# Kernel tuning notes

Measured on AMD Instinct MI355X. Metric: run time of the kernel, lower is better.

Reference implementation:

```python
import jax, jax.numpy as jnp
import numpy as np

REF_CHANNEL = 0
DIAG_EPS = 1e-7   # diag_loading coefficient
TIK_EPS = 1e-8    # additive eps in diagonal loading / trace denominator
MASK_EPS = 1e-15  # PSD mask-normalization eps


def _psd(spec, mask):
    # spec: (b, c, f, t) complex; mask: (b, f, t) real
    # PSD module: normalize mask over time, weight outer products, sum over t.
    m = mask / (mask.sum(axis=-1, keepdims=True) + MASK_EPS)
    return jnp.einsum('bcft,beft,bft->bfce', spec, spec.conj(), m.astype(spec.dtype))


def setup_inputs() -> dict:
    key = jax.random.key(0)
    k1, k2, k3, k4 = jax.random.split(key, 4)
    B, C, F, T = 4, 6, 257, 2000
    return {
        'spec_real': jax.random.normal(k1, (B, C, F, T), dtype=jnp.float32),
        'spec_imag': jax.random.normal(k2, (B, C, F, T), dtype=jnp.float32),
        'mask_s': jax.random.uniform(k3, (B, F, T), dtype=jnp.float32),
        'mask_n': jax.random.uniform(k4, (B, F, T), dtype=jnp.float32),
    }


def reference(spec_real, spec_imag, mask_s, mask_n):
    spec = spec_real + 1j * spec_imag                     # (b, c, f, t) complex64
    C = spec.shape[1]

    psd_s = _psd(spec, mask_s)                            # (b, f, c, c)
    psd_n = _psd(spec, mask_n)                            # (b, f, c, c)

    # Diagonal loading (Tikhonov regularization) of the noise PSD.
    tr_n = jnp.einsum('bfcc->bf', psd_n).real
    epsilon = jax.lax.stop_gradient(tr_n * DIAG_EPS + TIK_EPS)   # torch uses no_grad here
    psd_n = psd_n + epsilon[..., None, None] * jnp.eye(C, dtype=spec.dtype)

    # ref_channel solution: w = (psd_n^-1 psd_s) / trace(psd_n^-1 psd_s) @ u
    numerator = jnp.linalg.solve(psd_n, psd_s)            # (b, f, c, c)
    tr = jnp.einsum('bfcc->bf', numerator)
    ws = numerator / (tr[..., None, None] + TIK_EPS)
    w = ws[..., :, REF_CHANNEL]                           # one-hot u selects column -> (b, f, c)

    # enhanced = w^H Y
    enh = jnp.einsum('bfc,bcft->bft', w.conj(), spec)     # (b, f, t) complex
    return jnp.stack([enh.real, enh.imag], axis=-1)       # (b, f, t, 2) float32
```

## Files before the change

### kernel.cpp

```cpp
#include <hip/hip_runtime.h>

#define NB 4
#define NC 6
#define NF 257
#define NT 2000
#define NG (NB * NF)
#define NPAIR 15
#define NACC 74
#define NCHUNK 2
#define TCH (NT / NCHUNK)
#define NP4 (TCH / 4)
#define BLK 256
#define CS  (NF * NT)
#define CS4 (CS / 4)

typedef float nfloat4 __attribute__((ext_vector_type(4)));

template<int CTRL>
__device__ __forceinline__ float dpp_add(float v) {
    int s = __builtin_amdgcn_update_dpp(0, __builtin_bit_cast(int, v), CTRL, 0xF, 0xF, true);
    return v + __builtin_bit_cast(float, s);
}

__global__ __launch_bounds__(BLK, 4) void psd_kernel(
    const float* __restrict__ sr, const float* __restrict__ si,
    const float* __restrict__ ms, const float* __restrict__ mn,
    float* __restrict__ wsp)
{
    constexpr int PC[NPAIR] = {0,0,0,0,0,1,1,1,1,2,2,2,3,3,4};
    constexpr int PE[NPAIR] = {1,2,3,4,5,2,3,4,5,3,4,5,4,5,5};

    const int bx = blockIdx.x;
    const int g  = bx >> 1;
    const int b  = g / NF;
    const int f  = g - b * NF;
    const int tb = (bx & 1) * TCH;
    const int sbase = b * NC * CS + f * NT + tb;
    const int mbase = g * NT + tb;

    const float4* s4r = (const float4*)(sr + sbase);
    const float4* s4i = (const float4*)(si + sbase);
    const float4* m4s = (const float4*)(ms + mbase);
    const float4* m4n = (const float4*)(mn + mbase);

    float acc[NACC];
    #pragma unroll
    for (int i = 0; i < NACC; i++) acc[i] = 0.f;

    const bool act = threadIdx.x < NP4;
    const int  p   = act ? threadIdx.x : 0;
    {
        float wms[4], wmn[4], rr[NC][4], ii[NC][4];
        {
            const float4 t0 = m4s[p];
            wms[0] = t0.x; wms[1] = t0.y; wms[2] = t0.z; wms[3] = t0.w;
            const float4 t1 = m4n[p];
            wmn[0] = t1.x; wmn[1] = t1.y; wmn[2] = t1.z; wmn[3] = t1.w;
        }
        #pragma unroll
        for (int c = 0; c < NC; c++) {
            const float4 tr = s4r[c * CS4 + p];
            rr[c][0] = tr.x; rr[c][1] = tr.y; rr[c][2] = tr.z; rr[c][3] = tr.w;
            const float4 ti = s4i[c * CS4 + p];
            ii[c][0] = ti.x; ii[c][1] = ti.y; ii[c][2] = ti.z; ii[c][3] = ti.w;
        }
        if (!act) {
            #pragma unroll
            for (int k = 0; k < 4; k++) { wms[k] = 0.f; wmn[k] = 0.f; }
        }
        #pragma unroll
        for (int k = 0; k < 4; k++) { acc[72] += wms[k]; acc[73] += wmn[k]; }
        #pragma unroll
        for (int c = 0; c < NC; c++) {
            #pragma unroll
            for (int k = 0; k < 4; k++) {
                const float d = rr[c][k] * rr[c][k] + ii[c][k] * ii[c][k];
                acc[c]     += d * wms[k];
                acc[6 + c] += d * wmn[k];
            }
        }
        #pragma unroll
        for (int q = 0; q < NPAIR; q++) {
            const int c = PC[q], e = PE[q];
            #pragma unroll
            for (int k = 0; k < 4; k++) {
                const float cr = rr[c][k] * rr[e][k] + ii[c][k] * ii[e][k];
                const float ci = ii[c][k] * rr[e][k] - rr[c][k] * ii[e][k];
                acc[12 + 4 * q + 0] += cr * wms[k];
                acc[12 + 4 * q + 1] += ci * wms[k];
                acc[12 + 4 * q + 2] += cr * wmn[k];
                acc[12 + 4 * q + 3] += ci * wmn[k];
            }
        }
    }

    #pragma unroll
    for (int i = 0; i < NACC; i++) {
        float v = acc[i];
        v = dpp_add<0x118>(v);
        v = dpp_add<0x114>(v);
        v = dpp_add<0x112>(v);
        acc[i] = v;
    }

    __shared__ float red[32][NACC];
    const int lane16 = threadIdx.x & 15;
    const int ridx   = ((threadIdx.x >> 4) << 1) | (lane16 & 1);
    if (lane16 >= 14) {
        #pragma unroll
        for (int i = 0; i < NACC; i++) red[ridx][i] = acc[i];
    }
    __syncthreads();

    if (threadIdx.x < NACC) {
        float s = 0.f;
        #pragma unroll
        for (int r = 0; r < 32; r++) s += red[r][threadIdx.x];
        wsp[bx * NACC + threadIdx.x] = s;
    }
}

__global__ __launch_bounds__(64, 1) void solve_kernel(
    const float* __restrict__ wsp, float* __restrict__ wsw)
{
    const int gid = blockIdx.x * 64 + threadIdx.x;
    if (gid >= NG) return;

    constexpr int PC[NPAIR] = {0,0,0,0,0,1,1,1,1,2,2,2,3,3,4};
    constexpr int PE[NPAIR] = {1,2,3,4,5,2,3,4,5,3,4,5,4,5,5};
    constexpr int QIDX[NC][NC] = {
        {-1, 0, 1, 2, 3, 4},
        {-1,-1, 5, 6, 7, 8},
        {-1,-1,-1, 9,10,11},
        {-1,-1,-1,-1,12,13},
        {-1,-1,-1,-1,-1,14},
        {-1,-1,-1,-1,-1,-1}};

    const float* p0 = wsp + (2 * gid) * NACC;
    const float* p1 = p0 + NACC;
    float fin[NACC];
    #pragma unroll
    for (int i = 0; i < NACC; i++) fin[i] = p0[i] + p1[i];

    const float invS = 1.f / (fin[72] + 1e-15f);
    const float invN = 1.f / (fin[73] + 1e-15f);

    float Ar[NC][NC], Ai[NC][NC];
    #pragma unroll
    for (int c = 0; c < NC; c++) { Ar[c][c] = fin[6 + c] * invN; Ai[c][c] = 0.f; }
    #pragma unroll
    for (int q = 0; q < NPAIR; q++) {
        const int c = PC[q], e = PE[q];
        const float nre = fin[12 + 4 * q + 2] * invN;
        const float nim = fin[12 + 4 * q + 3] * invN;
        Ar[c][e] = nre;  Ai[c][e] = nim;
        Ar[e][c] = nre;  Ai[e][c] = -nim;
    }
    {
        float trn = 0.f;
        #pragma unroll
        for (int c = 0; c < NC; c++) trn += Ar[c][c];
        const float eps = trn * 1e-7f + 1e-8f;
        #pragma unroll
        for (int c = 0; c < NC; c++) Ar[c][c] += eps;
    }

    #pragma unroll
    for (int k = 0; k < NC; k++) {
        const float dr = Ar[k][k], di = Ai[k][k];
        const float idn = 1.f / (dr * dr + di * di);
        const float pr = dr * idn, pi = -di * idn;
        #pragma unroll
        for (int i = k + 1; i < NC; i++) {
            const float lr = Ar[i][k] * pr - Ai[i][k] * pi;
            const float li = Ar[i][k] * pi + Ai[i][k] * pr;
            Ar[i][k] = lr; Ai[i][k] = li;
            #pragma unroll
            for (int j = k + 1; j < NC; j++) {
                Ar[i][j] -= lr * Ar[k][j] - li * Ai[k][j];
                Ai[i][j] -= lr * Ai[k][j] + li * Ar[k][j];
            }
        }
    }

    float trr = 1e-8f, tri = 0.f;
    float w0r[NC], w0i[NC];
    #pragma unroll
    for (int j = 0; j < NC; j++) {
        float xr[NC], xi[NC];
        #pragma unroll
        for (int i = 0; i < NC; i++) {
            if (i == j)      { xr[i] = fin[j] * invS;                      xi[i] = 0.f; }
            else if (i < j)  { const int q = QIDX[i][j];
                               xr[i] = fin[12 + 4 * q] * invS;  xi[i] =  fin[13 + 4 * q] * invS; }
            else             { const int q = QIDX[j][i];
                               xr[i] = fin[12 + 4 * q] * invS;  xi[i] = -fin[13 + 4 * q] * invS; }
        }
        #pragma unroll
        for (int i = 1; i < NC; i++) {
            #pragma unroll
            for (int k = 0; k < NC - 1; k++) if (k < i) {
                xr[i] -= Ar[i][k] * xr[k] - Ai[i][k] * xi[k];
                xi[i] -= Ar[i][k] * xi[k] + Ai[i][k] * xr[k];
            }
        }
        #pragma unroll
        for (int i = NC - 1; i >= 0; i--) {
            #pragma unroll
            for (int k = 0; k < NC; k++) if (k > i) {
                xr[i] -= Ar[i][k] * xr[k] - Ai[i][k] * xi[k];
                xi[i] -= Ar[i][k] * xi[k] + Ai[i][k] * xr[k];
            }
            const float dr = Ar[i][i], di = Ai[i][i];
            const float idn = 1.f / (dr * dr + di * di);
            const float pr = dr * idn, pi = -di * idn;
            const float tr0 = xr[i] * pr - xi[i] * pi;
            xi[i] = xr[i] * pi + xi[i] * pr;
            xr[i] = tr0;
        }
        trr += xr[j]; tri += xi[j];
        if (j == 0) {
            #pragma unroll
            for (int i = 0; i < NC; i++) { w0r[i] = xr[i]; w0i[i] = xi[i]; }
        }
    }

    const float idn = 1.f / (trr * trr + tri * tri);
    #pragma unroll
    for (int c = 0; c < NC; c++) {
        const float wre = (w0r[c] * trr + w0i[c] * tri) * idn;
        const float wim = (w0i[c] * trr - w0r[c] * tri) * idn;
        wsw[gid * 12 + c]     = wre;
        wsw[gid * 12 + 6 + c] = -wim;
    }
}

__global__ __launch_bounds__(BLK) void apply_kernel(
    const float* __restrict__ sr, const float* __restrict__ si,
    const float* __restrict__ wsw, float* __restrict__ out)
{
    const int bx = blockIdx.x;
    const int g  = bx >> 1;
    const int b  = g / NF;
    const int f  = g - b * NF;
    const int tb = (bx & 1) * TCH;
    const int sbase = b * NC * CS + f * NT + tb;

    const float4* s4r = (const float4*)(sr + sbase);
    const float4* s4i = (const float4*)(si + sbase);

    float wr[NC], wi[NC];
    #pragma unroll
    for (int c = 0; c < NC; c++) {
        wr[c] = wsw[g * 12 + c];
        wi[c] = wsw[g * 12 + 6 + c];
    }

    nfloat4* o4 = (nfloat4*)(out + 2 * (g * NT + tb));

    const int p = threadIdx.x;
    if (p < NP4) {
        float rr[NC][4], ii[NC][4];
        #pragma unroll
        for (int c = 0; c < NC; c++) {
            const float4 tr = s4r[c * CS4 + p];
            rr[c][0] = tr.x; rr[c][1] = tr.y; rr[c][2] = tr.z; rr[c][3] = tr.w;
            const float4 ti = s4i[c * CS4 + p];
            ii[c][0] = ti.x; ii[c][1] = ti.y; ii[c][2] = ti.z; ii[c][3] = ti.w;
        }
        float er[4], ei[4];
        #pragma unroll
        for (int k = 0; k < 4; k++) {
            float a = 0.f, bb = 0.f;
            #pragma unroll
            for (int c = 0; c < NC; c++) {
                a  += wr[c] * rr[c][k] - wi[c] * ii[c][k];
                bb += wr[c] * ii[c][k] + wi[c] * rr[c][k];
            }
            er[k] = a; ei[k] = bb;
        }
        nfloat4 o0 = {er[0], ei[0], er[1], ei[1]};
        nfloat4 o1 = {er[2], ei[2], er[3], ei[3]};
        __builtin_nontemporal_store(o0, &o4[2 * p]);
        __builtin_nontemporal_store(o1, &o4[2 * p + 1]);
    }
}

extern "C" void kernel_launch(void* const* d_in, const int* in_sizes, int n_in,
                              void* d_out, int out_size, void* d_ws, size_t ws_size,
                              hipStream_t stream) {
    const float* sr = (const float*)d_in[0];
    const float* si = (const float*)d_in[1];
    const float* ms = (const float*)d_in[2];
    const float* mn = (const float*)d_in[3];
    float* out = (float*)d_out;

    float* wsp = (float*)d_ws;
    float* wsw = wsp + NG * NCHUNK * NACC;

    psd_kernel<<<NG * NCHUNK, BLK, 0, stream>>>(sr, si, ms, mn, wsp);
    solve_kernel<<<(NG + 63) / 64, 64, 0, stream>>>(wsp, wsw);
    apply_kernel<<<NG * NCHUNK, BLK, 0, stream>>>(sr, si, wsw, out);
}
```

Baseline: 201.2 us.

## Restructure PSD kernel to one wavefront per frequency with double-buffered loads

The PSD accumulation now launches one 64-thread wavefront per (batch, frequency) instead of two 256-thread blocks covering half the time axis each. Each lane iterates over 8 strided chunks with register double-buffering of the next chunk's loads. The shared-memory block reduction and __syncthreads are replaced by DPP plus cross-row shuffles, and two lanes write partial sums interleaved for the solve kernel. This removes the LDS reduction and the per-block launch overhead, but leaves 1028 small blocks of one wave each. That can limit occupancy and memory-level parallelism on a large GPU, and the double buffers raise register pressure.

Result: faster. 186.6 us (-7.2%).

```diff
diff --git a/kernel.cpp b/kernel.cpp
--- a/kernel.cpp
+++ b/kernel.cpp
@@ -7,6 +7,8 @@
 #define NG (NB * NF)
 #define NPAIR 15
 #define NACC 74
+#define NP4G (NT / 4)
+#define NIT 8
 #define NCHUNK 2
 #define TCH (NT / NCHUNK)
 #define NP4 (TCH / 4)
@@ -22,7 +24,7 @@
     return v + __builtin_bit_cast(float, s);
 }
 
-__global__ __launch_bounds__(BLK, 4) void psd_kernel(
+__global__ __launch_bounds__(64, 1) void psd_kernel(
     const float* __restrict__ sr, const float* __restrict__ si,
     const float* __restrict__ ms, const float* __restrict__ mn,
     float* __restrict__ wsp)
@@ -30,43 +32,52 @@
     constexpr int PC[NPAIR] = {0,0,0,0,0,1,1,1,1,2,2,2,3,3,4};
     constexpr int PE[NPAIR] = {1,2,3,4,5,2,3,4,5,3,4,5,4,5,5};
 
-    const int bx = blockIdx.x;
-    const int g  = bx >> 1;
+    const int g  = blockIdx.x;
     const int b  = g / NF;
     const int f  = g - b * NF;
-    const int tb = (bx & 1) * TCH;
-    const int sbase = b * NC * CS + f * NT + tb;
-    const int mbase = g * NT + tb;
+    const int sbase = b * NC * CS + f * NT;
+    const int mbase = g * NT;
 
     const float4* s4r = (const float4*)(sr + sbase);
     const float4* s4i = (const float4*)(si + sbase);
     const float4* m4s = (const float4*)(ms + mbase);
     const float4* m4n = (const float4*)(mn + mbase);
 
+    const int lane = threadIdx.x;
+
     float acc[NACC];
     #pragma unroll
     for (int i = 0; i < NACC; i++) acc[i] = 0.f;
 
-    const bool act = threadIdx.x < NP4;
-    const int  p   = act ? threadIdx.x : 0;
-    {
-        float wms[4], wmn[4], rr[NC][4], ii[NC][4];
-        {
-            const float4 t0 = m4s[p];
-            wms[0] = t0.x; wms[1] = t0.y; wms[2] = t0.z; wms[3] = t0.w;
-            const float4 t1 = m4n[p];
-            wmn[0] = t1.x; wmn[1] = t1.y; wmn[2] = t1.z; wmn[3] = t1.w;
-        }
+    float4 bm[2][2];
+    float4 brr[2][NC], bii[2][NC];
+
+    auto do_load = [&](int it, int u) {
+        const int praw = lane + 64 * it;
+        const int p = (praw < NP4G) ? praw : 0;
+        bm[u][0] = m4s[p];
+        bm[u][1] = m4n[p];
         #pragma unroll
         for (int c = 0; c < NC; c++) {
-            const float4 tr = s4r[c * CS4 + p];
-            rr[c][0] = tr.x; rr[c][1] = tr.y; rr[c][2] = tr.z; rr[c][3] = tr.w;
-            const float4 ti = s4i[c * CS4 + p];
-            ii[c][0] = ti.x; ii[c][1] = ti.y; ii[c][2] = ti.z; ii[c][3] = ti.w;
-        }
+            brr[u][c] = s4r[c * CS4 + p];
+            bii[u][c] = s4i[c * CS4 + p];
+        }
+    };
+
+    auto do_compute = [&](int it, int u) {
+        const bool act = (lane + 64 * it) < NP4G;
+        float wms[4], wmn[4];
+        wms[0] = bm[u][0].x; wms[1] = bm[u][0].y; wms[2] = bm[u][0].z; wms[3] = bm[u][0].w;
+        wmn[0] = bm[u][1].x; wmn[1] = bm[u][1].y; wmn[2] = bm[u][1].z; wmn[3] = bm[u][1].w;
         if (!act) {
             #pragma unroll
             for (int k = 0; k < 4; k++) { wms[k] = 0.f; wmn[k] = 0.f; }
+        }
+        float rr[NC][4], ii[NC][4];
+        #pragma unroll
+        for (int c = 0; c < NC; c++) {
+            rr[c][0] = brr[u][c].x; rr[c][1] = brr[u][c].y; rr[c][2] = brr[u][c].z; rr[c][3] = brr[u][c].w;
+            ii[c][0] = bii[u][c].x; ii[c][1] = bii[u][c].y; ii[c][2] = bii[u][c].z; ii[c][3] = bii[u][c].w;
         }
         #pragma unroll
         for (int k = 0; k < 4; k++) { acc[72] += wms[k]; acc[73] += wmn[k]; }
@@ -92,6 +103,13 @@
                 acc[12 + 4 * q + 3] += ci * wmn[k];
             }
         }
+    };
+
+    do_load(0, 0);
+    #pragma unroll
+    for (int it = 0; it < NIT; ++it) {
+        if (it + 1 < NIT) do_load(it + 1, (it + 1) & 1);
+        do_compute(it, it & 1);
     }
 
     #pragma unroll
@@ -100,23 +118,14 @@
         v = dpp_add<0x118>(v);
         v = dpp_add<0x114>(v);
         v = dpp_add<0x112>(v);
+        v += __shfl_xor(v, 16);
+        v += __shfl_xor(v, 32);
         acc[i] = v;
     }
-
-    __shared__ float red[32][NACC];
-    const int lane16 = threadIdx.x & 15;
-    const int ridx   = ((threadIdx.x >> 4) << 1) | (lane16 & 1);
-    if (lane16 >= 14) {
-        #pragma unroll
-        for (int i = 0; i < NACC; i++) red[ridx][i] = acc[i];
-    }
-    __syncthreads();
-
-    if (threadIdx.x < NACC) {
-        float s = 0.f;
-        #pragma unroll
-        for (int r = 0; r < 32; r++) s += red[r][threadIdx.x];
-        wsp[bx * NACC + threadIdx.x] = s;
+    if (lane == 14 || lane == 15) {
+        #pragma unroll
+        for (int i = 0; i < NACC; i++)
+            wsp[g * (2 * NACC) + 2 * i + (lane & 1)] = acc[i];
     }
 }
 
@@ -136,11 +145,10 @@
         {-1,-1,-1,-1,-1,14},
         {-1,-1,-1,-1,-1,-1}};
 
-    const float* p0 = wsp + (2 * gid) * NACC;
-    const float* p1 = p0 + NACC;
+    const float* pg = wsp + gid * (2 * NACC);
     float fin[NACC];
     #pragma unroll
-    for (int i = 0; i < NACC; i++) fin[i] = p0[i] + p1[i];
+    for (int i = 0; i < NACC; i++) fin[i] = pg[2 * i] + pg[2 * i + 1];
 
     const float invS = 1.f / (fin[72] + 1e-15f);
     const float invN = 1.f / (fin[73] + 1e-15f);
@@ -296,9 +304,9 @@
     float* out = (float*)d_out;
 
     float* wsp = (float*)d_ws;
-    float* wsw = wsp + NG * NCHUNK * NACC;
-
-    psd_kernel<<<NG * NCHUNK, BLK, 0, stream>>>(sr, si, ms, mn, wsp);
+    float* wsw = wsp + NG * (2 * NACC);
+
+    psd_kernel<<<NG, 64, 0, stream>>>(sr, si, ms, mn, wsp);
     solve_kernel<<<(NG + 63) / 64, 64, 0, stream>>>(wsp, wsw);
     apply_kernel<<<NG * NCHUNK, BLK, 0, stream>>>(sr, si, wsw, out);
 }
```
